# Kernel tuning notes

Hardware: AMD Instinct MI355X
Metric: run time of the kernel (lower is better)

## Reference

```python
import jax, jax.numpy as jnp
import numpy as np

IN_FEATURES = 512
OUT_FEATURES = 256
N = 2048

def setup_inputs() -> dict:
    key = jax.random.key(0)
    k1, k2, k3 = jax.random.split(key, 3)
    x = jax.random.normal(k1, (N, IN_FEATURES), dtype=jnp.float32)
    # kaiming_uniform_(a=sqrt(5)) -> uniform(-b, b) with b = sqrt(6/((1+5)*fan_in)) = 1/sqrt(fan_in)
    bound_w = 1.0 / np.sqrt(IN_FEATURES)
    weight = jax.random.uniform(k2, (OUT_FEATURES, IN_FEATURES), dtype=jnp.float32,
                                minval=-bound_w, maxval=bound_w)
    bound_b = 1.0 / np.sqrt(IN_FEATURES)
    bias = jax.random.uniform(k3, (OUT_FEATURES,), dtype=jnp.float32,
                              minval=-bound_b, maxval=bound_b)
    return {"x": x, "weight": weight, "bias": bias}

def reference(x, weight, bias):
    # MAM fully-connected (beta == 0 path):
    # prod[n, k, j] = x[n, k] * weight[j, k]
    # C[n, j] = max_k prod[n,k,j] + min_k prod[n,k,j] + bias[j]
    prod = x[:, :, None] * weight.T[None, :, :]   # [N, in, out]
    C = jnp.max(prod, axis=1) + jnp.min(prod, axis=1) + bias[None, :]
    return C
```

## Files before the change

### kernel.cpp

```cpp
#include <hip/hip_runtime.h>
#include <math.h>

#define NROWS 2048
#define INF_ 512
#define OUTF 256

__global__ __launch_bounds__(256) void mam_partial(
    const float* __restrict__ x, const float* __restrict__ w,
    float* __restrict__ pmax, float* __restrict__ pmin, int kLen)
{
    __shared__ __align__(16) float xs[32][68];
    __shared__ __align__(16) float wsh[32][68];

    const int t  = threadIdx.x;
    const int j0 = blockIdx.x * 64;
    const int n0 = blockIdx.y * 64;
    const int k0 = blockIdx.z * kLen;

    const int tx = t & 15;
    const int ty = t >> 4;

    float mx[4][4], mn[4][4];
#pragma unroll
    for (int i = 0; i < 4; ++i)
#pragma unroll
        for (int j = 0; j < 4; ++j) {
            mx[i][j] = -__builtin_inff();
            mn[i][j] =  __builtin_inff();
        }

    for (int c = 0; c < kLen; c += 32) {
        const int kc = k0 + c;
#pragma unroll
        for (int p = 0; p < 2; ++p) {
            int idx = t + p * 256;
            int n = idx >> 3, kv = idx & 7;
            float4 g = ((const float4*)(x + (size_t)(n0 + n) * INF_ + kc))[kv];
            xs[kv * 4 + 0][n] = g.x;
            xs[kv * 4 + 1][n] = g.y;
            xs[kv * 4 + 2][n] = g.z;
            xs[kv * 4 + 3][n] = g.w;
        }
#pragma unroll
        for (int p = 0; p < 2; ++p) {
            int idx = t + p * 256;
            int j = idx >> 3, kv = idx & 7;
            float4 g = ((const float4*)(w + (size_t)(j0 + j) * INF_ + kc))[kv];
            wsh[kv * 4 + 0][j] = g.x;
            wsh[kv * 4 + 1][j] = g.y;
            wsh[kv * 4 + 2][j] = g.z;
            wsh[kv * 4 + 3][j] = g.w;
        }
        __syncthreads();

#pragma unroll
        for (int kk = 0; kk < 32; ++kk) {
            float4 xv = *(const float4*)&xs[kk][ty * 4];
            float4 wv = *(const float4*)&wsh[kk][tx * 4];
            float xa[4] = {xv.x, xv.y, xv.z, xv.w};
            float wa[4] = {wv.x, wv.y, wv.z, wv.w};
#pragma unroll
            for (int i = 0; i < 4; ++i)
#pragma unroll
                for (int j = 0; j < 4; ++j) {
                    float p = xa[i] * wa[j];
                    mx[i][j] = fmaxf(mx[i][j], p);
                    mn[i][j] = fminf(mn[i][j], p);
                }
        }
        __syncthreads();
    }

    const size_t sOff = (size_t)blockIdx.z * NROWS * OUTF;
#pragma unroll
    for (int i = 0; i < 4; ++i) {
        size_t row = (size_t)(n0 + ty * 4 + i) * OUTF + j0 + tx * 4;
        float4 vmx = make_float4(mx[i][0], mx[i][1], mx[i][2], mx[i][3]);
        float4 vmn = make_float4(mn[i][0], mn[i][1], mn[i][2], mn[i][3]);
        *(float4*)(pmax + sOff + row) = vmx;
        *(float4*)(pmin + sOff + row) = vmn;
    }
}

__global__ __launch_bounds__(256) void mam_combine(
    const float* __restrict__ pmax, const float* __restrict__ pmin,
    const float* __restrict__ bias, float* __restrict__ out, int S)
{
    const int f = blockIdx.x * 256 + threadIdx.x;
    const int PLANE4 = NROWS * OUTF / 4;
    const float4* pm4 = (const float4*)pmax;
    const float4* pn4 = (const float4*)pmin;

    float4 a = pm4[f];
    float4 b = pn4[f];
    for (int s = 1; s < S; ++s) {
        float4 a2 = pm4[(size_t)s * PLANE4 + f];
        float4 b2 = pn4[(size_t)s * PLANE4 + f];
        a.x = fmaxf(a.x, a2.x); a.y = fmaxf(a.y, a2.y);
        a.z = fmaxf(a.z, a2.z); a.w = fmaxf(a.w, a2.w);
        b.x = fminf(b.x, b2.x); b.y = fminf(b.y, b2.y);
        b.z = fminf(b.z, b2.z); b.w = fminf(b.w, b2.w);
    }
    float4 bi = ((const float4*)bias)[f & 63];
    float4 o;
    o.x = a.x + b.x + bi.x;
    o.y = a.y + b.y + bi.y;
    o.z = a.z + b.z + bi.z;
    o.w = a.w + b.w + bi.w;
    ((float4*)out)[f] = o;
}

__global__ __launch_bounds__(256) void mam_naive(
    const float* __restrict__ x, const float* __restrict__ w,
    const float* __restrict__ bias, float* __restrict__ out)
{
    const int n = blockIdx.x;
    const int j = threadIdx.x;
    float mx = -__builtin_inff(), mn = __builtin_inff();
    for (int k = 0; k < INF_; ++k) {
        float p = x[(size_t)n * INF_ + k] * w[(size_t)j * INF_ + k];
        mx = fmaxf(mx, p);
        mn = fminf(mn, p);
    }
    out[(size_t)n * OUTF + j] = mx + mn + bias[j];
}

extern "C" void kernel_launch(void* const* d_in, const int* in_sizes, int n_in,
                              void* d_out, int out_size, void* d_ws, size_t ws_size,
                              hipStream_t stream) {
    const float* x    = (const float*)d_in[0];
    const float* w    = (const float*)d_in[1];
    const float* bias = (const float*)d_in[2];
    float* out = (float*)d_out;

    const size_t plane = (size_t)NROWS * OUTF * sizeof(float);
    int S;
    if      (ws_size >= 8 * plane) S = 4;
    else if (ws_size >= 4 * plane) S = 2;
    else if (ws_size >= 2 * plane) S = 1;
    else                           S = 0;

    if (S > 0) {
        float* pmax = (float*)d_ws;
        float* pmin = pmax + (size_t)S * NROWS * OUTF;
        dim3 grid(OUTF / 64, NROWS / 64, S);
        mam_partial<<<grid, 256, 0, stream>>>(x, w, pmax, pmin, INF_ / S);
        mam_combine<<<(NROWS * OUTF / 4) / 256, 256, 0, stream>>>(pmax, pmin, bias, out, S);
    } else {
        mam_naive<<<NROWS, 256, 0, stream>>>(x, w, bias, out);
    }
}
```

Measured before the change: 87.33 us.

## Replace split-K partial+combine with single fused kernel using direct global-to-LDS loads

Drops the split-K scheme, which wrote max/min partial planes to workspace and merged them in a second kernel. A single kernel now covers the full K range and adds the bias in its epilogue. It uses 64x32 output tiles, stages 256-wide K chunks into row-major padded LDS through global_load_lds async copies, and reads float4 along K. This removes the workspace round trip and the extra launch, at the cost of a smaller per-thread tile (4x2), more LDS per block, and fewer total blocks with no K split.

```diff
diff --git a/kernel.cpp b/kernel.cpp
--- a/kernel.cpp
+++ b/kernel.cpp
@@ -1,128 +1,93 @@
 #include <hip/hip_runtime.h>
 #include <math.h>
 
-#define NROWS 2048
-#define INF_ 512
-#define OUTF 256
+#define N_ 2048
+#define K_ 512
+#define J_ 256
+#define TN 64
+#define TJ 32
+#define BK 256
+#define RP 260
 
-__global__ __launch_bounds__(256) void mam_partial(
+typedef __attribute__((address_space(3))) float       lds_f;
+typedef const __attribute__((address_space(1))) float glb_f;
+
+__global__ __launch_bounds__(256) void mam_fused(
     const float* __restrict__ x, const float* __restrict__ w,
-    float* __restrict__ pmax, float* __restrict__ pmin, int kLen)
+    const float* __restrict__ bias, float* __restrict__ out)
 {
-    __shared__ __align__(16) float xs[32][68];
-    __shared__ __align__(16) float wsh[32][68];
+    __shared__ __align__(16) float xs[TN * RP];
+    __shared__ __align__(16) float wsh[TJ * RP];
 
-    const int t  = threadIdx.x;
-    const int j0 = blockIdx.x * 64;
-    const int n0 = blockIdx.y * 64;
-    const int k0 = blockIdx.z * kLen;
+    const int t    = threadIdx.x;
+    const int lane = t & 63;
+    const int wid  = t >> 6;
+    const int j0   = blockIdx.x * TJ;
+    const int n0   = blockIdx.y * TN;
+    const int tx   = t & 15;
+    const int ty   = t >> 4;
 
-    const int tx = t & 15;
-    const int ty = t >> 4;
-
-    float mx[4][4], mn[4][4];
+    float mx[4][2], mn[4][2];
 #pragma unroll
     for (int i = 0; i < 4; ++i)
 #pragma unroll
-        for (int j = 0; j < 4; ++j) {
+        for (int j = 0; j < 2; ++j) {
             mx[i][j] = -__builtin_inff();
             mn[i][j] =  __builtin_inff();
         }
 
-    for (int c = 0; c < kLen; c += 32) {
-        const int kc = k0 + c;
+    for (int kc = 0; kc < K_; kc += BK) {
 #pragma unroll
-        for (int p = 0; p < 2; ++p) {
-            int idx = t + p * 256;
-            int n = idx >> 3, kv = idx & 7;
-            float4 g = ((const float4*)(x + (size_t)(n0 + n) * INF_ + kc))[kv];
-            xs[kv * 4 + 0][n] = g.x;
-            xs[kv * 4 + 1][n] = g.y;
-            xs[kv * 4 + 2][n] = g.z;
-            xs[kv * 4 + 3][n] = g.w;
+        for (int r = 0; r < 16; ++r) {
+            const int row = wid * 16 + r;
+            __builtin_amdgcn_global_load_lds(
+                (glb_f*)(x + (size_t)(n0 + row) * K_ + kc + lane * 4),
+                (lds_f*)(xs + row * RP), 16, 0, 0);
         }
 #pragma unroll
-        for (int p = 0; p < 2; ++p) {
-            int idx = t + p * 256;
-            int j = idx >> 3, kv = idx & 7;
-            float4 g = ((const float4*)(w + (size_t)(j0 + j) * INF_ + kc))[kv];
-            wsh[kv * 4 + 0][j] = g.x;
-            wsh[kv * 4 + 1][j] = g.y;
-            wsh[kv * 4 + 2][j] = g.z;
-            wsh[kv * 4 + 3][j] = g.w;
+        for (int r = 0; r < 8; ++r) {
+            const int row = wid * 8 + r;
+            __builtin_amdgcn_global_load_lds(
+                (glb_f*)(w + (size_t)(j0 + row) * K_ + kc + lane * 4),
+                (lds_f*)(wsh + row * RP), 16, 0, 0);
         }
         __syncthreads();
 
-#pragma unroll
-        for (int kk = 0; kk < 32; ++kk) {
-            float4 xv = *(const float4*)&xs[kk][ty * 4];
-            float4 wv = *(const float4*)&wsh[kk][tx * 4];
-            float xa[4] = {xv.x, xv.y, xv.z, xv.w};
-            float wa[4] = {wv.x, wv.y, wv.z, wv.w};
+#pragma unroll 4
+        for (int kk = 0; kk < BK; kk += 4) {
+            float4 xv[4], wq[2];
 #pragma unroll
             for (int i = 0; i < 4; ++i)
+                xv[i] = *(const float4*)&xs[(ty * 4 + i) * RP + kk];
 #pragma unroll
-                for (int j = 0; j < 4; ++j) {
-                    float p = xa[i] * wa[j];
-                    mx[i][j] = fmaxf(mx[i][j], p);
-                    mn[i][j] = fminf(mn[i][j], p);
+            for (int j = 0; j < 2; ++j)
+                wq[j] = *(const float4*)&wsh[(tx * 2 + j) * RP + kk];
+#pragma unroll
+            for (int i = 0; i < 4; ++i) {
+                const float xa[4] = {xv[i].x, xv[i].y, xv[i].z, xv[i].w};
+#pragma unroll
+                for (int j = 0; j < 2; ++j) {
+                    const float wa[4] = {wq[j].x, wq[j].y, wq[j].z, wq[j].w};
+#pragma unroll
+                    for (int q = 0; q < 4; ++q) {
+                        const float p = xa[q] * wa[q];
+                        mx[i][j] = fmaxf(mx[i][j], p);
+                        mn[i][j] = fminf(mn[i][j], p);
+                    }
                 }
+            }
         }
         __syncthreads();
     }
 
-    const size_t sOff = (size_t)blockIdx.z * NROWS * OUTF;
+    const float2 bi = *(const float2*)&bias[j0 + tx * 2];
 #pragma unroll
     for (int i = 0; i < 4; ++i) {
-        size_t row = (size_t)(n0 + ty * 4 + i) * OUTF + j0 + tx * 4;
-        float4 vmx = make_float4(mx[i][0], mx[i][1], mx[i][2], mx[i][3]);
-        float4 vmn = make_float4(mn[i][0], mn[i][1], mn[i][2], mn[i][3]);
-        *(float4*)(pmax + sOff + row) = vmx;
-        *(float4*)(pmin + sOff + row) = vmn;
+        float2 o;
+        o.x = mx[i][0] + mn[i][0] + bi.x;
+        o.y = mx[i][1] + mn[i][1] + bi.y;
+        *(float2*)&out[(size_t)(n0 + ty * 4 + i) * J_ + j0 + tx * 2] = o;
     }
-}
-
-__global__ __launch_bounds__(256) void mam_combine(
-    const float* __restrict__ pmax, const float* __restrict__ pmin,
-    const float* __restrict__ bias, float* __restrict__ out, int S)
-{
-    const int f = blockIdx.x * 256 + threadIdx.x;
-    const int PLANE4 = NROWS * OUTF / 4;
-    const float4* pm4 = (const float4*)pmax;
-    const float4* pn4 = (const float4*)pmin;
-
-    float4 a = pm4[f];
-    float4 b = pn4[f];
-    for (int s = 1; s < S; ++s) {
-        float4 a2 = pm4[(size_t)s * PLANE4 + f];
-        float4 b2 = pn4[(size_t)s * PLANE4 + f];
-        a.x = fmaxf(a.x, a2.x); a.y = fmaxf(a.y, a2.y);
-        a.z = fmaxf(a.z, a2.z); a.w = fmaxf(a.w, a2.w);
-        b.x = fminf(b.x, b2.x); b.y = fminf(b.y, b2.y);
-        b.z = fminf(b.z, b2.z); b.w = fminf(b.w, b2.w);
-    }
-    float4 bi = ((const float4*)bias)[f & 63];
-    float4 o;
-    o.x = a.x + b.x + bi.x;
-    o.y = a.y + b.y + bi.y;
-    o.z = a.z + b.z + bi.z;
-    o.w = a.w + b.w + bi.w;
-    ((float4*)out)[f] = o;
-}
-
-__global__ __launch_bounds__(256) void mam_naive(
-    const float* __restrict__ x, const float* __restrict__ w,
-    const float* __restrict__ bias, float* __restrict__ out)
-{
-    const int n = blockIdx.x;
-    const int j = threadIdx.x;
-    float mx = -__builtin_inff(), mn = __builtin_inff();
-    for (int k = 0; k < INF_; ++k) {
-        float p = x[(size_t)n * INF_ + k] * w[(size_t)j * INF_ + k];
-        mx = fmaxf(mx, p);
-        mn = fminf(mn, p);
-    }
-    out[(size_t)n * OUTF + j] = mx + mn + bias[j];
 }
 
 extern "C" void kernel_launch(void* const* d_in, const int* in_sizes, int n_in,
@@ -133,20 +98,6 @@
     const float* bias = (const float*)d_in[2];
     float* out = (float*)d_out;
 
-    const size_t plane = (size_t)NROWS * OUTF * sizeof(float);
-    int S;
-    if      (ws_size >= 8 * plane) S = 4;
-    else if (ws_size >= 4 * plane) S = 2;
-    else if (ws_size >= 2 * plane) S = 1;
-    else                           S = 0;
-
-    if (S > 0) {
-        float* pmax = (float*)d_ws;
-        float* pmin = pmax + (size_t)S * NROWS * OUTF;
-        dim3 grid(OUTF / 64, NROWS / 64, S);
-        mam_partial<<<grid, 256, 0, stream>>>(x, w, pmax, pmin, INF_ / S);
-        mam_combine<<<(NROWS * OUTF / 4) / 256, 256, 0, stream>>>(pmax, pmin, bias, out, S);
-    } else {
-        mam_naive<<<NROWS, 256, 0, stream>>>(x, w, bias, out);
-    }
+    dim3 grid(J_ / TJ, N_ / TN);
+    mam_fused<<<grid, 256, 0, stream>>>(x, w, bias, out);
 }
```

Result: faster. 82.94 us (-5.0%).
